# Kernel optimization log

Measured on AMD Instinct MI355X. Metric: run time of the kernel, lower is better.

## Reference

```python
import jax, jax.numpy as jnp
import numpy as np

D = 64        # input_dim == hidden dims
D2 = 2 * D    # transformer model dim
N = 20000     # num_nodes
R = 24        # num_relation
S = 3         # history snapshots
E = 60000     # edges per snapshot
B = 8         # batch
K = 101       # candidates (1 pos + 100 neg)
HLEN = 50     # history length
NL_GNN = 2
NL_TF = 2
NH = 2        # attention heads
HD = D2 // NH


def setup_inputs() -> dict:
    key = jax.random.key(0)
    ks = list(jax.random.split(key, 40))
    nrm = lambda i, shape: jax.random.normal(ks[i], shape, jnp.float32) * 0.05
    inp = {}
    # embeddings / params
    inp["poi_emb"] = nrm(0, (N, D))
    inp["query_emb"] = nrm(1, (R, D))
    inp["gate_W"] = nrm(2, (D, D)); inp["gate_b"] = jnp.zeros((D,), jnp.float32)
    inp["gnn_rel"] = nrm(3, (NL_GNN, R, D))
    inp["gnn_W"] = nrm(4, (NL_GNN, 2 * D, D)); inp["gnn_b"] = jnp.zeros((NL_GNN, D), jnp.float32)
    inp["g_time_emb"] = nrm(5, (48, D))
    inp["g_lin_W"] = nrm(6, (D, D)); inp["g_lin_b"] = jnp.zeros((D,), jnp.float32)
    inp["tf_Wqkv"] = nrm(7, (NL_TF, D2, 3 * D2))
    inp["tf_Wo"] = nrm(8, (NL_TF, D2, D2))
    ln = jnp.stack([jnp.ones((NL_TF, D2), jnp.float32), jnp.zeros((NL_TF, D2), jnp.float32)], axis=1)
    inp["tf_ln1"] = ln; inp["tf_ln2"] = ln
    inp["tf_W1"] = nrm(9, (NL_TF, D2, 4 * D2)); inp["tf_b1"] = jnp.zeros((NL_TF, 4 * D2), jnp.float32)
    inp["tf_W2"] = nrm(10, (NL_TF, 4 * D2, D2)); inp["tf_b2"] = jnp.zeros((NL_TF, D2), jnp.float32)
    F_DIM = D + D2  # hidden_dims[-1] + 2*input_dim
    inp["mlp_W1"] = nrm(11, (F_DIM, F_DIM)); inp["mlp_b1"] = jnp.zeros((F_DIM,), jnp.float32)
    inp["mlp_W2"] = nrm(12, (F_DIM, 1)); inp["mlp_b2"] = jnp.zeros((1,), jnp.float32)
    inp["history_time_encoding"] = nrm(13, (B, HLEN, D2))
    # graph / index inputs
    inp["edge_src"] = jax.random.randint(ks[14], (S, E), 0, N)
    inp["edge_dst"] = jax.random.randint(ks[15], (S, E), 0, N)
    inp["edge_type"] = jax.random.randint(ks[16], (S, E), 0, R)
    inp["h_index"] = jax.random.randint(ks[17], (B,), 0, N)
    inp["r_index"] = jax.random.randint(ks[18], (B,), 0, R)
    inp["t_index"] = jax.random.randint(ks[19], (B, K), 0, N)
    inp["history_poi"] = jax.random.randint(ks[20], (B, HLEN), 0, N)
    inp["g_time"] = jax.random.randint(ks[21], (S,), 0, 48)
    return inp


def _layer_norm(x, scale, bias):
    m = x.mean(-1, keepdims=True)
    v = ((x - m) ** 2).mean(-1, keepdims=True)
    return (x - m) * jax.lax.rsqrt(v + 1e-5) * scale + bias


def reference(poi_emb, query_emb, gate_W, gate_b, gnn_rel, gnn_W, gnn_b,
              g_time_emb, g_lin_W, g_lin_b,
              tf_Wqkv, tf_Wo, tf_ln1, tf_W1, tf_b1, tf_W2, tf_b2, tf_ln2,
              mlp_W1, mlp_b1, mlp_W2, mlp_b2,
              history_time_encoding,
              edge_src, edge_dst, edge_type, h_index, r_index, t_index,
              history_poi, g_time):
    query = query_emb[r_index]  # [B, D]  (r_index constant across candidates)
    output = jnp.zeros((B, N, D), poi_emb.dtype)
    for s in range(S):  # temporal snapshot loop (memory_update per snapshot)
        src, dst, et = edge_src[s], edge_dst[s], edge_type[s]
        # scatter_add of poi embeddings over both endpoints; identical per batch row
        poi_node = jnp.concatenate([src, dst])  # [2E]
        init_one = jax.ops.segment_sum(poi_emb[poi_node], poi_node, num_segments=N)  # [N, D]
        init = jnp.broadcast_to(init_one[None], (B, N, D))
        if s > 0:
            gate = jax.nn.sigmoid(output @ gate_W + gate_b)  # sigmoid gating vs prior state
            init = init * gate + (1.0 - gate) * output
        x = init
        for l in range(NL_GNN):  # PathAggNet stack: transe message + scatter-sum + linear
            msg = x[:, src] + gnn_rel[l][et][None]  # [B, E, D]
            agg = jnp.zeros((B, N, D), x.dtype).at[:, dst].add(msg)  # [B, N, D]
            x = jax.nn.relu(jnp.concatenate([agg, init], axis=-1) @ gnn_W[l] + gnn_b[l])
        output = x
        query = (query + g_time_emb[g_time[s]][None]) @ g_lin_W + g_lin_b
    feature = output  # [B, N, D]
    r_emb = jnp.broadcast_to(query[:, None], (B, N, D))
    final_feature = jnp.concatenate([feature, r_emb], axis=-1)  # [B, N, 2D]
    # gather history POI features + time encoding -> transformer encoder
    poi_idx = jnp.broadcast_to(history_poi[..., None], (B, HLEN, D2))
    xseq = jnp.take_along_axis(final_feature, poi_idx, axis=1) + history_time_encoding  # [B, HLEN, 2D]
    for l in range(NL_TF):
        qkv = xseq @ tf_Wqkv[l]  # [B, HLEN, 3*D2]
        q, k, v = jnp.split(qkv, 3, axis=-1)
        split_heads = lambda t: t.reshape(B, HLEN, NH, HD).transpose(0, 2, 1, 3)
        q, k, v = split_heads(q), split_heads(k), split_heads(v)
        att = jax.nn.softmax(jnp.einsum('bnqd,bnkd->bnqk', q, k) / jnp.sqrt(jnp.float32(HD)), axis=-1)
        o = jnp.einsum('bnqk,bnkd->bnqd', att, v).transpose(0, 2, 1, 3).reshape(B, HLEN, D2) @ tf_Wo[l]
        xseq = _layer_norm(xseq + o, tf_ln1[l, 0], tf_ln1[l, 1])
        ff = jax.nn.relu(xseq @ tf_W1[l] + tf_b1[l]) @ tf_W2[l] + tf_b2[l]
        xseq = _layer_norm(xseq + ff, tf_ln2[l, 0], tf_ln2[l, 1])
    feature_label = xseq.mean(axis=1, keepdims=True)  # [B, 1, 2D]
    t_idx = jnp.broadcast_to(t_index[..., None], (B, K, D))
    feature_t = jnp.take_along_axis(feature, t_idx, axis=1)  # [B, K, D]
    feature_t = jnp.concatenate([feature_t, jnp.broadcast_to(feature_label, (B, K, D2))], axis=-1)
    hmid = jax.nn.relu(feature_t @ mlp_W1 + mlp_b1)
    score = (hmid @ mlp_W2 + mlp_b2).squeeze(-1)  # [B, K]
    return score
```

## Files before the change

### kernel.cpp

```cpp
#include <hip/hip_runtime.h>
#include <hip/hip_bf16.h>
#include <math.h>

#define DD   64
#define DD2  128
#define NN   20000
#define RR   24
#define SS   3
#define EE   60000
#define BB   8
#define KK   101
#define HLENN 50
#define MROWS 20024

__global__ void hist_kernel(const int* __restrict__ src, const int* __restrict__ dst,
                            int* __restrict__ hist, int* __restrict__ deg) {
    int s = blockIdx.y;
    int e = blockIdx.x * 256 + threadIdx.x;
    if (e < EE) {
        int d0 = dst[s * EE + e], s0 = src[s * EE + e];
        atomicAdd(&hist[s * NN + d0], 1);
        atomicAdd(&deg[s * NN + d0], 1);
        atomicAdd(&deg[s * NN + s0], 1);
    }
}

__global__ void scan_kernel(const int* __restrict__ hist, int* __restrict__ rowptr,
                            int* __restrict__ cursor) {
    int s = blockIdx.x, t = threadIdx.x;
    const int* h = hist + s * NN;
    int* rp = rowptr + s * (NN + 1);
    int* cur = cursor + s * NN;
    __shared__ int sp[1024];
    int base = t * 20, sum = 0;
    for (int i = 0; i < 20; ++i) { int idx = base + i; if (idx < NN) sum += h[idx]; }
    sp[t] = sum;
    __syncthreads();
    for (int off = 1; off < 1024; off <<= 1) {
        int v = (t >= off) ? sp[t - off] : 0;
        __syncthreads();
        sp[t] += v;
        __syncthreads();
    }
    int run = sp[t] - sum;
    for (int i = 0; i < 20; ++i) {
        int idx = base + i;
        if (idx < NN) { rp[idx] = run; cur[idx] = run; run += h[idx]; }
    }
    if (t == 1023) rp[NN] = sp[1023];
}

__global__ void place_kernel(const int* __restrict__ src, const int* __restrict__ dst,
                             const int* __restrict__ et, int* __restrict__ cursor,
                             int* __restrict__ colp) {
    int s = blockIdx.y;
    int e = blockIdx.x * 256 + threadIdx.x;
    if (e < EE) {
        int d0 = dst[s * EE + e];
        int pos = atomicAdd(&cursor[s * NN + d0], 1);
        colp[s * EE + pos] = src[s * EE + e] | (et[s * EE + e] << 16);
    }
}

__global__ void init_kernel(const float* __restrict__ poi, const int* __restrict__ deg,
                            const float* __restrict__ gate_W, const float* __restrict__ gate_b,
                            const float* __restrict__ xprev, float* __restrict__ initb,
                            int use_gate) {
    __shared__ float sW[64][64];
    __shared__ float srow[4][64];
    int li = threadIdx.x >> 6, d = threadIdx.x & 63;
    int node = blockIdx.x * 4 + li;
    if (use_gate) {
        for (int i = threadIdx.x; i < 64 * 64; i += 256) sW[i >> 6][i & 63] = gate_W[i];
    }
    float iv = (float)deg[node] * poi[node * 64 + d];
    if (use_gate) {
        float ov = xprev[node * 64 + d];
        srow[li][d] = ov;
        __syncthreads();
        float acc = gate_b[d];
        #pragma unroll
        for (int k = 0; k < 64; ++k) acc += srow[li][k] * sW[k][d];
        float g = 1.f / (1.f + expf(-acc));
        iv = iv * g + (1.f - g) * ov;
    }
    initb[node * 64 + d] = iv;
}

__global__ void gemm64_kernel(const float* __restrict__ A0a, const float* __restrict__ Ar_a,
                              const float* __restrict__ Ba, float* __restrict__ Ca,
                              const float* __restrict__ A0b, const float* __restrict__ Ar_b,
                              const float* __restrict__ Bb, float* __restrict__ Cb) {
    const float* A0 = blockIdx.y ? A0b : A0a;
    const float* Ar = blockIdx.y ? Ar_b : Ar_a;
    const float* B  = blockIdx.y ? Bb  : Ba;
    float* C        = blockIdx.y ? Cb  : Ca;
    __shared__ float sA[64][68];
    __shared__ float sB[64][68];
    int tid = threadIdx.x;
    int row0 = blockIdx.x * 64;
    for (int i = tid; i < 64 * 16; i += 256) {
        int r = i >> 4, cq = i & 15;
        int row = row0 + r;
        float4 v = make_float4(0.f, 0.f, 0.f, 0.f);
        if (row < NN)        v = *(const float4*)(A0 + (size_t)row * 64 + cq * 4);
        else if (row < MROWS) v = *(const float4*)(Ar + (size_t)(row - NN) * 64 + cq * 4);
        *(float4*)&sA[r][cq * 4] = v;
        if (i < 64 * 16) {
            float4 w = *(const float4*)(B + (size_t)r * 64 + cq * 4);
            *(float4*)&sB[r][cq * 4] = w;
        }
    }
    __syncthreads();
    int tr = tid >> 4, tc = tid & 15;
    float acc[4][4] = {{0.f}};
    #pragma unroll 16
    for (int k = 0; k < 64; ++k) {
        float4 b4 = *(const float4*)&sB[k][tc * 4];
        float a0 = sA[tr * 4 + 0][k];
        float a1 = sA[tr * 4 + 1][k];
        float a2 = sA[tr * 4 + 2][k];
        float a3 = sA[tr * 4 + 3][k];
        acc[0][0] += a0 * b4.x; acc[0][1] += a0 * b4.y; acc[0][2] += a0 * b4.z; acc[0][3] += a0 * b4.w;
        acc[1][0] += a1 * b4.x; acc[1][1] += a1 * b4.y; acc[1][2] += a1 * b4.z; acc[1][3] += a1 * b4.w;
        acc[2][0] += a2 * b4.x; acc[2][1] += a2 * b4.y; acc[2][2] += a2 * b4.z; acc[2][3] += a2 * b4.w;
        acc[3][0] += a3 * b4.x; acc[3][1] += a3 * b4.y; acc[3][2] += a3 * b4.z; acc[3][3] += a3 * b4.w;
    }
    #pragma unroll
    for (int i = 0; i < 4; ++i) {
        int row = row0 + tr * 4 + i;
        if (row < MROWS) {
            float4 o = make_float4(acc[i][0], acc[i][1], acc[i][2], acc[i][3]);
            *(float4*)(C + (size_t)row * 64 + tc * 4) = o;
        }
    }
}

__global__ void fin_kernel(const float* __restrict__ y, const float* __restrict__ z,
                           const int* __restrict__ rowptr, const int* __restrict__ colp,
                           const float* __restrict__ bias, float* __restrict__ xout) {
    __shared__ float srelW[24][64];
    int tid = threadIdx.x;
    for (int i = tid; i < 24 * 64; i += 256) srelW[i >> 6][i & 63] = y[NN * 64 + i];
    int d = tid & 63, w = tid >> 6;
    float bb = bias[d];
    __syncthreads();
    int base = blockIdx.x * 16 + w * 4;
    for (int n = 0; n < 4; ++n) {
        int node = base + n;
        float acc = z[node * 64 + d] + bb;
        int e0 = rowptr[node], e1 = rowptr[node + 1];
        for (int e = e0; e < e1; ++e) {
            int pack = colp[e];
            acc += y[(size_t)(pack & 0xFFFF) * 64 + d] + srelW[pack >> 16][d];
        }
        xout[node * 64 + d] = fmaxf(acc, 0.f);
    }
}

__global__ void query_kernel(const float* __restrict__ query_emb, const int* __restrict__ r_index,
                             const float* __restrict__ g_time_emb, const int* __restrict__ g_time,
                             const float* __restrict__ g_lin_W, const float* __restrict__ g_lin_b,
                             float* __restrict__ query) {
    __shared__ float sW[64][64];
    __shared__ float sq[8][64];
    int b = threadIdx.x >> 6;
    int d = threadIdx.x & 63;
    for (int i = threadIdx.x; i < 64 * 64; i += 512) sW[i >> 6][i & 63] = g_lin_W[i];
    float q = query_emb[r_index[b] * 64 + d];
    for (int s = 0; s < SS; ++s) {
        float t = q + g_time_emb[g_time[s] * 64 + d];
        sq[b][d] = t;
        __syncthreads();
        float acc = g_lin_b[d];
        #pragma unroll
        for (int k = 0; k < 64; ++k) acc += sq[b][k] * sW[k][d];
        q = acc;
        __syncthreads();
    }
    query[b * 64 + d] = q;
}

__global__ void xseq_kernel(const float* __restrict__ feature, const float* __restrict__ query,
                            const int* __restrict__ history_poi, const float* __restrict__ hte,
                            float* __restrict__ xseq) {
    int idx = blockIdx.x * 256 + threadIdx.x;
    if (idx >= BB * HLENN * DD2) return;
    int c = idx & 127;
    int bt = idx >> 7;
    int b = bt / HLENN, t = bt % HLENN;
    float v = (c < 64) ? feature[history_poi[b * HLENN + t] * 64 + c]
                       : query[b * 64 + (c - 64)];
    xseq[idx] = v + hte[idx];
}

__global__ void qkv4_kernel(const float* __restrict__ xseq, const float* __restrict__ Wqkv,
                            float* __restrict__ qkvb) {
    __shared__ float sx[4][128];
    int tid = threadIdx.x;
    int row0 = blockIdx.x * 4;
    for (int i = tid; i < 512; i += 384) sx[i >> 7][i & 127] = xseq[row0 * 128 + i];
    __syncthreads();
    float a0 = 0.f, a1 = 0.f, a2 = 0.f, a3 = 0.f;
    #pragma unroll 8
    for (int k = 0; k < 128; ++k) {
        float w = Wqkv[k * 384 + tid];
        a0 += sx[0][k] * w; a1 += sx[1][k] * w; a2 += sx[2][k] * w; a3 += sx[3][k] * w;
    }
    qkvb[(row0 + 0) * 384 + tid] = a0;
    qkvb[(row0 + 1) * 384 + tid] = a1;
    qkvb[(row0 + 2) * 384 + tid] = a2;
    qkvb[(row0 + 3) * 384 + tid] = a3;
}

__global__ void attn_kernel(const float* __restrict__ qkv, float* __restrict__ attnout) {
    int b = blockIdx.x >> 1, h = blockIdx.x & 1;
    __shared__ float sq[HLENN][64], sk[HLENN][64], sv[HLENN][64];
    __shared__ float ss[HLENN][HLENN];
    for (int i = threadIdx.x; i < HLENN * 64; i += 256) {
        int t = i >> 6, d = i & 63;
        const float* base = qkv + (size_t)(b * HLENN + t) * 384 + h * 64 + d;
        sq[t][d] = base[0];
        sk[t][d] = base[128];
        sv[t][d] = base[256];
    }
    __syncthreads();
    for (int p = threadIdx.x; p < HLENN * HLENN; p += 256) {
        int i = p / HLENN, j = p % HLENN;
        float acc = 0.f;
        #pragma unroll 8
        for (int d = 0; d < 64; ++d) acc += sq[i][d] * sk[j][d];
        ss[i][j] = acc * 0.125f;
    }
    __syncthreads();
    if (threadIdx.x < HLENN) {
        int i = threadIdx.x;
        float m = -1e30f;
        for (int j = 0; j < HLENN; ++j) m = fmaxf(m, ss[i][j]);
        float sum = 0.f;
        for (int j = 0; j < HLENN; ++j) { float e = expf(ss[i][j] - m); ss[i][j] = e; sum += e; }
        float inv = 1.f / sum;
        for (int j = 0; j < HLENN; ++j) ss[i][j] *= inv;
    }
    __syncthreads();
    for (int p = threadIdx.x; p < HLENN * 64; p += 256) {
        int i = p >> 6, d = p & 63;
        float acc = 0.f;
        for (int j = 0; j < HLENN; ++j) acc += ss[i][j] * sv[j][d];
        attnout[(size_t)(b * HLENN + i) * 128 + h * 64 + d] = acc;
    }
}

__global__ void addLN4_kernel(const float* __restrict__ aout, const float* __restrict__ Wo,
                              const float* __restrict__ ln, float* __restrict__ xseq) {
    __shared__ float sa[4][128];
    __shared__ float sred[4][128];
    int tid = threadIdx.x;
    int r = tid >> 7, c = tid & 127;
    int row0 = blockIdx.x * 4;
    sa[r][c] = aout[(row0 + r) * 128 + c];
    __syncthreads();
    float acc = xseq[(row0 + r) * 128 + c];
    #pragma unroll 8
    for (int k = 0; k < 128; ++k) acc += sa[r][k] * Wo[k * 128 + c];
    sred[r][c] = acc; __syncthreads();
    for (int off = 64; off > 0; off >>= 1) { if (c < off) sred[r][c] += sred[r][c + off]; __syncthreads(); }
    float mean = sred[r][0] * (1.f / 128.f);
    __syncthreads();
    float dx = acc - mean;
    sred[r][c] = dx * dx; __syncthreads();
    for (int off = 64; off > 0; off >>= 1) { if (c < off) sred[r][c] += sred[r][c + off]; __syncthreads(); }
    float var = sred[r][0] * (1.f / 128.f);
    xseq[(row0 + r) * 128 + c] = dx * rsqrtf(var + 1e-5f) * ln[c] + ln[128 + c];
}

__global__ void ffLN4_kernel(const float* __restrict__ xin, const float* __restrict__ W1,
                             const float* __restrict__ b1, const float* __restrict__ W2,
                             const float* __restrict__ b2, const float* __restrict__ ln,
                             float* __restrict__ xout) {
    __shared__ float sx[4][128];
    __shared__ float sh[4][512];
    __shared__ float spart[4][4][128];
    __shared__ float sred[4][128];
    int tid = threadIdx.x;
    int row0 = blockIdx.x * 4;
    { int r = tid >> 7, c = tid & 127; sx[r][c] = xin[(row0 + r) * 128 + c]; }
    __syncthreads();
    {
        float bb = b1[tid];
        float a0 = bb, a1 = bb, a2 = bb, a3 = bb;
        #pragma unroll 8
        for (int k = 0; k < 128; ++k) {
            float w = W1[k * 512 + tid];
            a0 += sx[0][k] * w; a1 += sx[1][k] * w; a2 += sx[2][k] * w; a3 += sx[3][k] * w;
        }
        sh[0][tid] = fmaxf(a0, 0.f); sh[1][tid] = fmaxf(a1, 0.f);
        sh[2][tid] = fmaxf(a2, 0.f); sh[3][tid] = fmaxf(a3, 0.f);
    }
    __syncthreads();
    int kc = tid >> 7, c = tid & 127;
    float p0 = 0.f, p1 = 0.f, p2 = 0.f, p3 = 0.f;
    #pragma unroll 8
    for (int kk = 0; kk < 128; ++kk) {
        int k = kc * 128 + kk;
        float w = W2[k * 128 + c];
        p0 += sh[0][k] * w; p1 += sh[1][k] * w; p2 += sh[2][k] * w; p3 += sh[3][k] * w;
    }
    spart[kc][0][c] = p0; spart[kc][1][c] = p1; spart[kc][2][c] = p2; spart[kc][3][c] = p3;
    __syncthreads();
    int r = kc;
    float acc = b2[c] + spart[0][r][c] + spart[1][r][c] + spart[2][r][c] + spart[3][r][c] + sx[r][c];
    sred[r][c] = acc; __syncthreads();
    for (int off = 64; off > 0; off >>= 1) { if (c < off) sred[r][c] += sred[r][c + off]; __syncthreads(); }
    float mean = sred[r][0] * (1.f / 128.f);
    __syncthreads();
    float dx = acc - mean;
    sred[r][c] = dx * dx; __syncthreads();
    for (int off = 64; off > 0; off >>= 1) { if (c < off) sred[r][c] += sred[r][c + off]; __syncthreads(); }
    float var = sred[r][0] * (1.f / 128.f);
    xout[(row0 + r) * 128 + c] = dx * rsqrtf(var + 1e-5f) * ln[c] + ln[128 + c];
}

__global__ void mean_kernel(const float* __restrict__ xseq, float* __restrict__ flabel) {
    int i = blockIdx.x * 256 + threadIdx.x;
    if (i >= BB * 128) return;
    int b = i >> 7, c = i & 127;
    float s = 0.f;
    for (int t = 0; t < HLENN; ++t) s += xseq[(b * HLENN + t) * 128 + c];
    flabel[i] = s * (1.f / HLENN);
}

__global__ void score_kernel(const float* __restrict__ feature, const float* __restrict__ flabel,
                             const int* __restrict__ t_index,
                             const float* __restrict__ W1, const float* __restrict__ b1,
                             const float* __restrict__ W2, const float* __restrict__ b2,
                             float* __restrict__ score) {
    int b = blockIdx.x / KK, k = blockIdx.x % KK;
    __shared__ float sf[192];
    __shared__ float sred[192];
    int j = threadIdx.x;
    int t = t_index[b * KK + k];
    sf[j] = (j < 64) ? feature[t * 64 + j] : flabel[b * 128 + (j - 64)];
    __syncthreads();
    float acc = b1[j];
    #pragma unroll 8
    for (int i = 0; i < 192; ++i) acc += sf[i] * W1[i * 192 + j];
    float h = fmaxf(acc, 0.f);
    sred[j] = h * W2[j];
    __syncthreads();
    if (j < 64) sred[j] += sred[j + 64] + sred[j + 128];
    __syncthreads();
    for (int off = 32; off > 0; off >>= 1) { if (j < off) sred[j] += sred[j + off]; __syncthreads(); }
    if (j == 0) score[b * KK + k] = sred[0] + b2[0];
}

extern "C" void kernel_launch(void* const* d_in, const int* in_sizes, int n_in,
                              void* d_out, int out_size, void* d_ws, size_t ws_size,
                              hipStream_t stream) {
    const float* poi_emb   = (const float*)d_in[0];
    const float* query_emb = (const float*)d_in[1];
    const float* gate_W    = (const float*)d_in[2];
    const float* gate_b    = (const float*)d_in[3];
    const float* gnn_rel   = (const float*)d_in[4];
    const float* gnn_W     = (const float*)d_in[5];
    const float* gnn_b     = (const float*)d_in[6];
    const float* g_time_emb= (const float*)d_in[7];
    const float* g_lin_W   = (const float*)d_in[8];
    const float* g_lin_b   = (const float*)d_in[9];
    const float* tf_Wqkv   = (const float*)d_in[10];
    const float* tf_Wo     = (const float*)d_in[11];
    const float* tf_ln1    = (const float*)d_in[12];
    const float* tf_ln2    = (const float*)d_in[13];
    const float* tf_W1     = (const float*)d_in[14];
    const float* tf_b1     = (const float*)d_in[15];
    const float* tf_W2     = (const float*)d_in[16];
    const float* tf_b2     = (const float*)d_in[17];
    const float* mlp_W1    = (const float*)d_in[18];
    const float* mlp_b1    = (const float*)d_in[19];
    const float* mlp_W2    = (const float*)d_in[20];
    const float* mlp_b2    = (const float*)d_in[21];
    const float* hte       = (const float*)d_in[22];
    const int* edge_src    = (const int*)d_in[23];
    const int* edge_dst    = (const int*)d_in[24];
    const int* edge_type   = (const int*)d_in[25];
    const int* r_index     = (const int*)d_in[27];
    const int* t_index     = (const int*)d_in[28];
    const int* history_poi = (const int*)d_in[29];
    const int* g_time      = (const int*)d_in[30];

    float* ws = (float*)d_ws;
    float* xA    = ws;
    float* xB    = xA + 1280000;
    float* initb = xB + 1280000;
    float* y     = initb + 1280000;
    float* z     = y + 20032 * 64;
    float* query = z + 20032 * 64;
    float* xseq  = query + 512;
    float* qkvb  = xseq + 51200;
    float* aout  = qkvb + 153600;
    float* flab  = aout + 51200;
    int* hist    = (int*)(flab + 1024);
    int* deg     = hist + 3 * NN;
    int* rowptr  = deg + 3 * NN;
    int* cursor  = rowptr + 3 * (NN + 1);
    int* colp    = cursor + 3 * NN;

    hipMemsetAsync(hist, 0, 2 * 3 * NN * sizeof(int), stream);
    {
        dim3 g((EE + 255) / 256, 3);
        hist_kernel<<<g, 256, 0, stream>>>(edge_src, edge_dst, hist, deg);
        scan_kernel<<<3, 1024, 0, stream>>>(hist, rowptr, cursor);
        place_kernel<<<g, 256, 0, stream>>>(edge_src, edge_dst, edge_type, cursor, colp);
    }

    for (int s = 0; s < SS; ++s) {
        const int* rp = rowptr + s * (NN + 1);
        const int* cp = colp + s * EE;
        init_kernel<<<NN / 4, 256, 0, stream>>>(poi_emb, deg + s * NN, gate_W, gate_b,
                                                xA, initb, s > 0 ? 1 : 0);
        const float* Wt0 = gnn_W;
        const float* Wb0 = gnn_W + 64 * 64;
        const float* Wt1 = gnn_W + 128 * 64;
        const float* Wb1 = gnn_W + 128 * 64 + 64 * 64;
        const float* rel0 = gnn_rel;
        const float* rel1 = gnn_rel + 24 * 64;
        dim3 gg(313, 2);
        gemm64_kernel<<<gg, 256, 0, stream>>>(initb, rel0, Wt0, y,
                                              initb, rel0, Wb0, z);
        fin_kernel<<<NN / 16, 256, 0, stream>>>(y, z, rp, cp, gnn_b, xB);
        gemm64_kernel<<<gg, 256, 0, stream>>>(xB, rel1, Wt1, y,
                                              initb, rel1, Wb1, z);
        fin_kernel<<<NN / 16, 256, 0, stream>>>(y, z, rp, cp, gnn_b + 64, xA);
    }

    query_kernel<<<1, 512, 0, stream>>>(query_emb, r_index, g_time_emb, g_time,
                                        g_lin_W, g_lin_b, query);
    xseq_kernel<<<(BB * HLENN * 128 + 255) / 256, 256, 0, stream>>>(xA, query, history_poi, hte, xseq);

    for (int l = 0; l < 2; ++l) {
        qkv4_kernel<<<BB * HLENN / 4, 384, 0, stream>>>(xseq, tf_Wqkv + l * 128 * 384, qkvb);
        attn_kernel<<<BB * 2, 256, 0, stream>>>(qkvb, aout);
        addLN4_kernel<<<BB * HLENN / 4, 512, 0, stream>>>(aout, tf_Wo + l * 128 * 128,
                                                          tf_ln1 + l * 256, xseq);
        ffLN4_kernel<<<BB * HLENN / 4, 512, 0, stream>>>(xseq, tf_W1 + l * 128 * 512,
                                                         tf_b1 + l * 512, tf_W2 + l * 512 * 128,
                                                         tf_b2 + l * 128, tf_ln2 + l * 256, xseq);
    }

    mean_kernel<<<(BB * 128 + 255) / 256, 256, 0, stream>>>(xseq, flab);
    score_kernel<<<BB * KK, 192, 0, stream>>>(xA, flab, t_index,
                                              mlp_W1, mlp_b1, mlp_W2, mlp_b2, (float*)d_out);
}
```

Measured before the change: 526.0 us.

## Fuse CSR build, GNN init+GEMM, aggregation+GEMM, and transformer into few kernels

CSR construction now runs as a single per-snapshot kernel that uses an LDS histogram, scan and placement, replacing the memset and three launches. The gate/init step is fused with the dual y/z GEMM, and the first aggregation is fused with the next layer's GEMM, so intermediate node features are not round-tripped through global memory. The whole transformer, including the query chain, xseq build, two layers and the mean, runs in one kernel with one block per batch element. This cuts launch count and global traffic, at the cost of very low parallelism: the transformer uses only 8 blocks and the CSR build only 3 blocks with 1024 threads each.

```diff
diff --git a/kernel.cpp b/kernel.cpp
--- a/kernel.cpp
+++ b/kernel.cpp
@@ -13,27 +13,25 @@
 #define HLENN 50
 #define MROWS 20024
 
-__global__ void hist_kernel(const int* __restrict__ src, const int* __restrict__ dst,
-                            int* __restrict__ hist, int* __restrict__ deg) {
-    int s = blockIdx.y;
-    int e = blockIdx.x * 256 + threadIdx.x;
-    if (e < EE) {
-        int d0 = dst[s * EE + e], s0 = src[s * EE + e];
-        atomicAdd(&hist[s * NN + d0], 1);
-        atomicAdd(&deg[s * NN + d0], 1);
-        atomicAdd(&deg[s * NN + s0], 1);
-    }
-}
-
-__global__ void scan_kernel(const int* __restrict__ hist, int* __restrict__ rowptr,
-                            int* __restrict__ cursor) {
+__global__ __launch_bounds__(1024) void csr_kernel(
+        const int* __restrict__ src, const int* __restrict__ dst,
+        const int* __restrict__ et,
+        int* __restrict__ rowptr,
+        int* __restrict__ colp,
+        int* __restrict__ deg) {
+    __shared__ int lh[NN];
+    __shared__ int sp[1024];
     int s = blockIdx.x, t = threadIdx.x;
-    const int* h = hist + s * NN;
+    const int* ps = src + s * EE;
+    const int* pd = dst + s * EE;
+    const int* pt = et + s * EE;
     int* rp = rowptr + s * (NN + 1);
-    int* cur = cursor + s * NN;
-    __shared__ int sp[1024];
+    for (int i = t; i < NN; i += 1024) lh[i] = 0;
+    __syncthreads();
+    for (int e = t; e < EE; e += 1024) atomicAdd(&lh[pd[e]], 1);
+    __syncthreads();
     int base = t * 20, sum = 0;
-    for (int i = 0; i < 20; ++i) { int idx = base + i; if (idx < NN) sum += h[idx]; }
+    for (int i = 0; i < 20; ++i) { int idx = base + i; if (idx < NN) sum += lh[idx]; }
     sp[t] = sum;
     __syncthreads();
     for (int off = 1; off < 1024; off <<= 1) {
@@ -45,302 +43,352 @@
     int run = sp[t] - sum;
     for (int i = 0; i < 20; ++i) {
         int idx = base + i;
-        if (idx < NN) { rp[idx] = run; cur[idx] = run; run += h[idx]; }
+        if (idx < NN) { rp[idx] = run; int c = lh[idx]; lh[idx] = run; run += c; }
     }
     if (t == 1023) rp[NN] = sp[1023];
-}
-
-__global__ void place_kernel(const int* __restrict__ src, const int* __restrict__ dst,
-                             const int* __restrict__ et, int* __restrict__ cursor,
-                             int* __restrict__ colp) {
-    int s = blockIdx.y;
-    int e = blockIdx.x * 256 + threadIdx.x;
-    if (e < EE) {
-        int d0 = dst[s * EE + e];
-        int pos = atomicAdd(&cursor[s * NN + d0], 1);
-        colp[s * EE + pos] = src[s * EE + e] | (et[s * EE + e] << 16);
-    }
-}
-
-__global__ void init_kernel(const float* __restrict__ poi, const int* __restrict__ deg,
-                            const float* __restrict__ gate_W, const float* __restrict__ gate_b,
-                            const float* __restrict__ xprev, float* __restrict__ initb,
-                            int use_gate) {
-    __shared__ float sW[64][64];
+    __syncthreads();
+    for (int e = t; e < EE; e += 1024) {
+        int pos = atomicAdd(&lh[pd[e]], 1);
+        colp[s * EE + pos] = ps[e] | (pt[e] << 16);
+    }
+    __syncthreads();
+    for (int i = t; i < NN; i += 1024) lh[i] = 0;
+    __syncthreads();
+    for (int e = t; e < EE; e += 1024) atomicAdd(&lh[ps[e]], 1);
+    __syncthreads();
+    for (int i = t; i < NN; i += 1024)
+        deg[s * NN + i] = lh[i] + (rp[i + 1] - rp[i]);
+}
+
+__global__ __launch_bounds__(256) void initgemm_kernel(
+        const float* __restrict__ poi, const int* __restrict__ deg,
+        const float* __restrict__ gate_W, const float* __restrict__ gate_b,
+        const float* __restrict__ xprev, const float* __restrict__ rel,
+        const float* __restrict__ W,
+        float* __restrict__ initb, float* __restrict__ y, float* __restrict__ z,
+        int use_gate) {
+    __shared__ float sGW[64][64];
+    __shared__ float sA[64][68];
+    __shared__ float sBt[64][68];
+    __shared__ float sBb[64][68];
     __shared__ float srow[4][64];
-    int li = threadIdx.x >> 6, d = threadIdx.x & 63;
-    int node = blockIdx.x * 4 + li;
+    int tid = threadIdx.x;
+    int li = tid >> 6, d = tid & 63;
+    int row0 = blockIdx.x * 64;
     if (use_gate) {
-        for (int i = threadIdx.x; i < 64 * 64; i += 256) sW[i >> 6][i & 63] = gate_W[i];
-    }
-    float iv = (float)deg[node] * poi[node * 64 + d];
-    if (use_gate) {
-        float ov = xprev[node * 64 + d];
-        srow[li][d] = ov;
-        __syncthreads();
-        float acc = gate_b[d];
+        for (int i = tid; i < 64 * 64; i += 256) sGW[i >> 6][i & 63] = gate_W[i];
+        __syncthreads();
+    }
+    float gb = use_gate ? gate_b[d] : 0.f;
+    for (int it = 0; it < 16; ++it) {
+        int rl = it * 4 + li;
+        int row = row0 + rl;
+        float iv;
+        if (row < NN)           iv = (float)deg[row] * poi[(size_t)row * 64 + d];
+        else if (row < MROWS)   iv = rel[(row - NN) * 64 + d];
+        else                    iv = 0.f;
+        if (use_gate) {
+            float ov = (row < NN) ? xprev[(size_t)row * 64 + d] : 0.f;
+            srow[li][d] = ov;
+            __syncthreads();
+            float acc = gb;
+            #pragma unroll
+            for (int k = 0; k < 64; ++k) acc += srow[li][k] * sGW[k][d];
+            float g = 1.f / (1.f + expf(-acc));
+            if (row < NN) iv = iv * g + (1.f - g) * ov;
+            __syncthreads();
+        }
+        sA[rl][d] = iv;
+        if (row < NN) initb[(size_t)row * 64 + d] = iv;
+    }
+    for (int i = tid; i < 64 * 64; i += 256) {
+        sBt[i >> 6][i & 63] = W[i];
+        sBb[i >> 6][i & 63] = W[64 * 64 + i];
+    }
+    __syncthreads();
+    int tr = tid >> 4, tc = tid & 15;
+    float accY[4][4] = {{0.f}}, accZ[4][4] = {{0.f}};
+    #pragma unroll 16
+    for (int k = 0; k < 64; ++k) {
+        float4 bt = *(const float4*)&sBt[k][tc * 4];
+        float4 bz = *(const float4*)&sBb[k][tc * 4];
         #pragma unroll
-        for (int k = 0; k < 64; ++k) acc += srow[li][k] * sW[k][d];
-        float g = 1.f / (1.f + expf(-acc));
-        iv = iv * g + (1.f - g) * ov;
-    }
-    initb[node * 64 + d] = iv;
-}
-
-__global__ void gemm64_kernel(const float* __restrict__ A0a, const float* __restrict__ Ar_a,
-                              const float* __restrict__ Ba, float* __restrict__ Ca,
-                              const float* __restrict__ A0b, const float* __restrict__ Ar_b,
-                              const float* __restrict__ Bb, float* __restrict__ Cb) {
-    const float* A0 = blockIdx.y ? A0b : A0a;
-    const float* Ar = blockIdx.y ? Ar_b : Ar_a;
-    const float* B  = blockIdx.y ? Bb  : Ba;
-    float* C        = blockIdx.y ? Cb  : Ca;
+        for (int i = 0; i < 4; ++i) {
+            float a = sA[tr * 4 + i][k];
+            accY[i][0] += a * bt.x; accY[i][1] += a * bt.y; accY[i][2] += a * bt.z; accY[i][3] += a * bt.w;
+            accZ[i][0] += a * bz.x; accZ[i][1] += a * bz.y; accZ[i][2] += a * bz.z; accZ[i][3] += a * bz.w;
+        }
+    }
+    #pragma unroll
+    for (int i = 0; i < 4; ++i) {
+        int row = row0 + tr * 4 + i;
+        if (row < MROWS) {
+            *(float4*)(y + (size_t)row * 64 + tc * 4) = make_float4(accY[i][0], accY[i][1], accY[i][2], accY[i][3]);
+            *(float4*)(z + (size_t)row * 64 + tc * 4) = make_float4(accZ[i][0], accZ[i][1], accZ[i][2], accZ[i][3]);
+        }
+    }
+}
+
+__global__ __launch_bounds__(256) void fingemm_kernel(
+        const float* __restrict__ y, const float* __restrict__ z,
+        const int* __restrict__ rp, const int* __restrict__ cp,
+        const float* __restrict__ bias0, const float* __restrict__ rel1,
+        const float* __restrict__ W1,
+        const float* __restrict__ initb,
+        float* __restrict__ y2, float* __restrict__ z2) {
+    __shared__ float srelW[24][64];
     __shared__ float sA[64][68];
-    __shared__ float sB[64][68];
+    __shared__ float sAi[64][68];
+    __shared__ float sBt[64][68];
+    __shared__ float sBb[64][68];
     int tid = threadIdx.x;
+    int li = tid >> 6, d = tid & 63;
     int row0 = blockIdx.x * 64;
+    for (int i = tid; i < 24 * 64; i += 256) srelW[i >> 6][i & 63] = y[(size_t)NN * 64 + i];
+    for (int i = tid; i < 64 * 64; i += 256) {
+        sBt[i >> 6][i & 63] = W1[i];
+        sBb[i >> 6][i & 63] = W1[64 * 64 + i];
+    }
     for (int i = tid; i < 64 * 16; i += 256) {
         int r = i >> 4, cq = i & 15;
         int row = row0 + r;
         float4 v = make_float4(0.f, 0.f, 0.f, 0.f);
-        if (row < NN)        v = *(const float4*)(A0 + (size_t)row * 64 + cq * 4);
-        else if (row < MROWS) v = *(const float4*)(Ar + (size_t)(row - NN) * 64 + cq * 4);
-        *(float4*)&sA[r][cq * 4] = v;
-        if (i < 64 * 16) {
-            float4 w = *(const float4*)(B + (size_t)r * 64 + cq * 4);
-            *(float4*)&sB[r][cq * 4] = w;
-        }
+        if (row < NN) v = *(const float4*)(initb + (size_t)row * 64 + cq * 4);
+        *(float4*)&sAi[r][cq * 4] = v;
+    }
+    __syncthreads();
+    float bb0 = bias0[d];
+    for (int it = 0; it < 16; ++it) {
+        int rl = it * 4 + li;
+        int row = row0 + rl;
+        float val = 0.f;
+        if (row < NN) {
+            float acc = z[(size_t)row * 64 + d] + bb0;
+            int e0 = rp[row], e1 = rp[row + 1];
+            for (int e = e0; e < e1; ++e) {
+                int pack = cp[e];
+                acc += y[(size_t)(pack & 0xFFFF) * 64 + d] + srelW[pack >> 16][d];
+            }
+            val = fmaxf(acc, 0.f);
+        } else if (row < MROWS) {
+            val = rel1[(row - NN) * 64 + d];
+        }
+        sA[rl][d] = val;
     }
     __syncthreads();
     int tr = tid >> 4, tc = tid & 15;
-    float acc[4][4] = {{0.f}};
+    float accY[4][4] = {{0.f}}, accZ[4][4] = {{0.f}};
     #pragma unroll 16
     for (int k = 0; k < 64; ++k) {
-        float4 b4 = *(const float4*)&sB[k][tc * 4];
-        float a0 = sA[tr * 4 + 0][k];
-        float a1 = sA[tr * 4 + 1][k];
-        float a2 = sA[tr * 4 + 2][k];
-        float a3 = sA[tr * 4 + 3][k];
-        acc[0][0] += a0 * b4.x; acc[0][1] += a0 * b4.y; acc[0][2] += a0 * b4.z; acc[0][3] += a0 * b4.w;
-        acc[1][0] += a1 * b4.x; acc[1][1] += a1 * b4.y; acc[1][2] += a1 * b4.z; acc[1][3] += a1 * b4.w;
-        acc[2][0] += a2 * b4.x; acc[2][1] += a2 * b4.y; acc[2][2] += a2 * b4.z; acc[2][3] += a2 * b4.w;
-        acc[3][0] += a3 * b4.x; acc[3][1] += a3 * b4.y; acc[3][2] += a3 * b4.z; acc[3][3] += a3 * b4.w;
+        float4 bt = *(const float4*)&sBt[k][tc * 4];
+        float4 bz = *(const float4*)&sBb[k][tc * 4];
+        #pragma unroll
+        for (int i = 0; i < 4; ++i) {
+            float a  = sA[tr * 4 + i][k];
+            float ai = sAi[tr * 4 + i][k];
+            accY[i][0] += a * bt.x;  accY[i][1] += a * bt.y;  accY[i][2] += a * bt.z;  accY[i][3] += a * bt.w;
+            accZ[i][0] += ai * bz.x; accZ[i][1] += ai * bz.y; accZ[i][2] += ai * bz.z; accZ[i][3] += ai * bz.w;
+        }
     }
     #pragma unroll
     for (int i = 0; i < 4; ++i) {
         int row = row0 + tr * 4 + i;
         if (row < MROWS) {
-            float4 o = make_float4(acc[i][0], acc[i][1], acc[i][2], acc[i][3]);
-            *(float4*)(C + (size_t)row * 64 + tc * 4) = o;
-        }
-    }
-}
-
-__global__ void fin_kernel(const float* __restrict__ y, const float* __restrict__ z,
-                           const int* __restrict__ rowptr, const int* __restrict__ colp,
-                           const float* __restrict__ bias, float* __restrict__ xout) {
+            *(float4*)(y2 + (size_t)row * 64 + tc * 4) = make_float4(accY[i][0], accY[i][1], accY[i][2], accY[i][3]);
+            *(float4*)(z2 + (size_t)row * 64 + tc * 4) = make_float4(accZ[i][0], accZ[i][1], accZ[i][2], accZ[i][3]);
+        }
+    }
+}
+
+__global__ __launch_bounds__(256) void fin_kernel(
+        const float* __restrict__ y, const float* __restrict__ z,
+        const int* __restrict__ rowptr, const int* __restrict__ colp,
+        const float* __restrict__ bias, float* __restrict__ xout) {
     __shared__ float srelW[24][64];
     int tid = threadIdx.x;
-    for (int i = tid; i < 24 * 64; i += 256) srelW[i >> 6][i & 63] = y[NN * 64 + i];
+    for (int i = tid; i < 24 * 64; i += 256) srelW[i >> 6][i & 63] = y[(size_t)NN * 64 + i];
     int d = tid & 63, w = tid >> 6;
     float bb = bias[d];
     __syncthreads();
     int base = blockIdx.x * 16 + w * 4;
     for (int n = 0; n < 4; ++n) {
         int node = base + n;
-        float acc = z[node * 64 + d] + bb;
+        float acc = z[(size_t)node * 64 + d] + bb;
         int e0 = rowptr[node], e1 = rowptr[node + 1];
         for (int e = e0; e < e1; ++e) {
             int pack = colp[e];
             acc += y[(size_t)(pack & 0xFFFF) * 64 + d] + srelW[pack >> 16][d];
         }
-        xout[node * 64 + d] = fmaxf(acc, 0.f);
-    }
-}
-
-__global__ void query_kernel(const float* __restrict__ query_emb, const int* __restrict__ r_index,
-                             const float* __restrict__ g_time_emb, const int* __restrict__ g_time,
-                             const float* __restrict__ g_lin_W, const float* __restrict__ g_lin_b,
-                             float* __restrict__ query) {
-    __shared__ float sW[64][64];
-    __shared__ float sq[8][64];
-    int b = threadIdx.x >> 6;
-    int d = threadIdx.x & 63;
-    for (int i = threadIdx.x; i < 64 * 64; i += 512) sW[i >> 6][i & 63] = g_lin_W[i];
-    float q = query_emb[r_index[b] * 64 + d];
+        xout[(size_t)node * 64 + d] = fmaxf(acc, 0.f);
+    }
+}
+
+__global__ __launch_bounds__(512) void tf_kernel(
+        const float* __restrict__ feature, const float* __restrict__ query_emb,
+        const int* __restrict__ r_index, const float* __restrict__ g_time_emb,
+        const int* __restrict__ g_time, const float* __restrict__ g_lin_W,
+        const float* __restrict__ g_lin_b, const int* __restrict__ history_poi,
+        const float* __restrict__ hte,
+        const float* __restrict__ tf_Wqkv, const float* __restrict__ tf_Wo,
+        const float* __restrict__ tf_ln1, const float* __restrict__ tf_ln2,
+        const float* __restrict__ tf_W1, const float* __restrict__ tf_b1,
+        const float* __restrict__ tf_W2, const float* __restrict__ tf_b2,
+        float* __restrict__ flab) {
+    __shared__ float sxseq[HLENN][128];
+    __shared__ float sbig[25600];
+    __shared__ float ss[2][HLENN][HLENN];
+    __shared__ float sq[64], sq2[64];
+    __shared__ float smean[HLENN], svar[HLENN];
+    int b = blockIdx.x, tid = threadIdx.x;
+    if (tid < 64) sq2[tid] = query_emb[r_index[b] * 64 + tid];
+    __syncthreads();
     for (int s = 0; s < SS; ++s) {
-        float t = q + g_time_emb[g_time[s] * 64 + d];
-        sq[b][d] = t;
-        __syncthreads();
-        float acc = g_lin_b[d];
+        if (tid < 64) sq[tid] = sq2[tid] + g_time_emb[g_time[s] * 64 + tid];
+        __syncthreads();
+        float acc = 0.f;
+        if (tid < 64) {
+            acc = g_lin_b[tid];
+            #pragma unroll 8
+            for (int k = 0; k < 64; ++k) acc += sq[k] * g_lin_W[k * 64 + tid];
+        }
+        __syncthreads();
+        if (tid < 64) sq2[tid] = acc;
+        __syncthreads();
+    }
+    for (int p = tid; p < HLENN * 128; p += 512) {
+        int t = p >> 7, c = p & 127;
+        float v = (c < 64) ? feature[(size_t)history_poi[b * HLENN + t] * 64 + c]
+                           : sq2[c - 64];
+        sxseq[t][c] = v + hte[(b * HLENN + t) * 128 + c];
+    }
+    __syncthreads();
+    for (int l = 0; l < 2; ++l) {
+        const float* Wqkv = tf_Wqkv + l * 128 * 384;
+        const float* Wo   = tf_Wo   + l * 128 * 128;
+        const float* W1   = tf_W1   + l * 128 * 512;
+        const float* b1   = tf_b1   + l * 512;
+        const float* W2   = tf_W2   + l * 512 * 128;
+        const float* b2   = tf_b2   + l * 128;
+        const float* ln1  = tf_ln1  + l * 256;
+        const float* ln2  = tf_ln2  + l * 256;
+        for (int p = tid; p < HLENN * 384; p += 512) {
+            int t = p / 384, j = p % 384;
+            float acc = 0.f;
+            #pragma unroll 8
+            for (int k = 0; k < 128; ++k) acc += sxseq[t][k] * Wqkv[k * 384 + j];
+            sbig[t * 384 + j] = acc;
+        }
+        __syncthreads();
+        for (int p = tid; p < 2 * HLENN * HLENN; p += 512) {
+            int h = p / 2500, r = (p / 50) % 50, j = p % 50;
+            float acc = 0.f;
+            #pragma unroll 8
+            for (int k = 0; k < 64; ++k)
+                acc += sbig[r * 384 + h * 64 + k] * sbig[j * 384 + 128 + h * 64 + k];
+            ss[h][r][j] = acc * 0.125f;
+        }
+        __syncthreads();
+        if (tid < 2 * HLENN) {
+            int h = tid / HLENN, r = tid % HLENN;
+            float m = -1e30f;
+            for (int j = 0; j < HLENN; ++j) m = fmaxf(m, ss[h][r][j]);
+            float sum = 0.f;
+            for (int j = 0; j < HLENN; ++j) { float e = expf(ss[h][r][j] - m); ss[h][r][j] = e; sum += e; }
+            float inv = 1.f / sum;
+            for (int j = 0; j < HLENN; ++j) ss[h][r][j] *= inv;
+        }
+        __syncthreads();
+        for (int p = tid; p < HLENN * 128; p += 512) {
+            int t = p >> 7, c = p & 127, h = c >> 6, cc = c & 63;
+            float acc = 0.f;
+            for (int j = 0; j < HLENN; ++j)
+                acc += ss[h][t][j] * sbig[j * 384 + 256 + h * 64 + cc];
+            sbig[19200 + p] = acc;
+        }
+        __syncthreads();
+        for (int p = tid; p < HLENN * 128; p += 512) {
+            int t = p >> 7, c = p & 127;
+            float acc = sxseq[t][c];
+            #pragma unroll 8
+            for (int k = 0; k < 128; ++k) acc += sbig[19200 + t * 128 + k] * Wo[k * 128 + c];
+            sbig[p] = acc;
+        }
+        __syncthreads();
+        if (tid < HLENN) {
+            float m = 0.f;
+            for (int k = 0; k < 128; ++k) m += sbig[tid * 128 + k];
+            m *= (1.f / 128.f);
+            float v = 0.f;
+            for (int k = 0; k < 128; ++k) { float dx = sbig[tid * 128 + k] - m; v += dx * dx; }
+            smean[tid] = m; svar[tid] = v * (1.f / 128.f);
+        }
+        __syncthreads();
+        for (int p = tid; p < HLENN * 128; p += 512) {
+            int t = p >> 7, c = p & 127;
+            sxseq[t][c] = (sbig[p] - smean[t]) * rsqrtf(svar[t] + 1e-5f) * ln1[c] + ln1[128 + c];
+        }
+        __syncthreads();
+        for (int p = tid; p < HLENN * 512; p += 512) {
+            int t = p >> 9, j = p & 511;
+            float acc = b1[j];
+            #pragma unroll 8
+            for (int k = 0; k < 128; ++k) acc += sxseq[t][k] * W1[k * 512 + j];
+            sbig[p] = fmaxf(acc, 0.f);
+        }
+        __syncthreads();
+        float r2[13];
         #pragma unroll
-        for (int k = 0; k < 64; ++k) acc += sq[b][k] * sW[k][d];
-        q = acc;
-        __syncthreads();
-    }
-    query[b * 64 + d] = q;
-}
-
-__global__ void xseq_kernel(const float* __restrict__ feature, const float* __restrict__ query,
-                            const int* __restrict__ history_poi, const float* __restrict__ hte,
-                            float* __restrict__ xseq) {
-    int idx = blockIdx.x * 256 + threadIdx.x;
-    if (idx >= BB * HLENN * DD2) return;
-    int c = idx & 127;
-    int bt = idx >> 7;
-    int b = bt / HLENN, t = bt % HLENN;
-    float v = (c < 64) ? feature[history_poi[b * HLENN + t] * 64 + c]
-                       : query[b * 64 + (c - 64)];
-    xseq[idx] = v + hte[idx];
-}
-
-__global__ void qkv4_kernel(const float* __restrict__ xseq, const float* __restrict__ Wqkv,
-                            float* __restrict__ qkvb) {
-    __shared__ float sx[4][128];
-    int tid = threadIdx.x;
-    int row0 = blockIdx.x * 4;
-    for (int i = tid; i < 512; i += 384) sx[i >> 7][i & 127] = xseq[row0 * 128 + i];
-    __syncthreads();
-    float a0 = 0.f, a1 = 0.f, a2 = 0.f, a3 = 0.f;
-    #pragma unroll 8
-    for (int k = 0; k < 128; ++k) {
-        float w = Wqkv[k * 384 + tid];
-        a0 += sx[0][k] * w; a1 += sx[1][k] * w; a2 += sx[2][k] * w; a3 += sx[3][k] * w;
-    }
-    qkvb[(row0 + 0) * 384 + tid] = a0;
-    qkvb[(row0 + 1) * 384 + tid] = a1;
-    qkvb[(row0 + 2) * 384 + tid] = a2;
-    qkvb[(row0 + 3) * 384 + tid] = a3;
-}
-
-__global__ void attn_kernel(const float* __restrict__ qkv, float* __restrict__ attnout) {
-    int b = blockIdx.x >> 1, h = blockIdx.x & 1;
-    __shared__ float sq[HLENN][64], sk[HLENN][64], sv[HLENN][64];
-    __shared__ float ss[HLENN][HLENN];
-    for (int i = threadIdx.x; i < HLENN * 64; i += 256) {
-        int t = i >> 6, d = i & 63;
-        const float* base = qkv + (size_t)(b * HLENN + t) * 384 + h * 64 + d;
-        sq[t][d] = base[0];
-        sk[t][d] = base[128];
-        sv[t][d] = base[256];
-    }
-    __syncthreads();
-    for (int p = threadIdx.x; p < HLENN * HLENN; p += 256) {
-        int i = p / HLENN, j = p % HLENN;
-        float acc = 0.f;
-        #pragma unroll 8
-        for (int d = 0; d < 64; ++d) acc += sq[i][d] * sk[j][d];
-        ss[i][j] = acc * 0.125f;
-    }
-    __syncthreads();
-    if (threadIdx.x < HLENN) {
-        int i = threadIdx.x;
-        float m = -1e30f;
-        for (int j = 0; j < HLENN; ++j) m = fmaxf(m, ss[i][j]);
-        float sum = 0.f;
-        for (int j = 0; j < HLENN; ++j) { float e = expf(ss[i][j] - m); ss[i][j] = e; sum += e; }
-        float inv = 1.f / sum;
-        for (int j = 0; j < HLENN; ++j) ss[i][j] *= inv;
-    }
-    __syncthreads();
-    for (int p = threadIdx.x; p < HLENN * 64; p += 256) {
-        int i = p >> 6, d = p & 63;
-        float acc = 0.f;
-        for (int j = 0; j < HLENN; ++j) acc += ss[i][j] * sv[j][d];
-        attnout[(size_t)(b * HLENN + i) * 128 + h * 64 + d] = acc;
-    }
-}
-
-__global__ void addLN4_kernel(const float* __restrict__ aout, const float* __restrict__ Wo,
-                              const float* __restrict__ ln, float* __restrict__ xseq) {
-    __shared__ float sa[4][128];
-    __shared__ float sred[4][128];
-    int tid = threadIdx.x;
-    int r = tid >> 7, c = tid & 127;
-    int row0 = blockIdx.x * 4;
-    sa[r][c] = aout[(row0 + r) * 128 + c];
-    __syncthreads();
-    float acc = xseq[(row0 + r) * 128 + c];
-    #pragma unroll 8
-    for (int k = 0; k < 128; ++k) acc += sa[r][k] * Wo[k * 128 + c];
-    sred[r][c] = acc; __syncthreads();
-    for (int off = 64; off > 0; off >>= 1) { if (c < off) sred[r][c] += sred[r][c + off]; __syncthreads(); }
-    float mean = sred[r][0] * (1.f / 128.f);
-    __syncthreads();
-    float dx = acc - mean;
-    sred[r][c] = dx * dx; __syncthreads();
-    for (int off = 64; off > 0; off >>= 1) { if (c < off) sred[r][c] += sred[r][c + off]; __syncthreads(); }
-    float var = sred[r][0] * (1.f / 128.f);
-    xseq[(row0 + r) * 128 + c] = dx * rsqrtf(var + 1e-5f) * ln[c] + ln[128 + c];
-}
-
-__global__ void ffLN4_kernel(const float* __restrict__ xin, const float* __restrict__ W1,
-                             const float* __restrict__ b1, const float* __restrict__ W2,
-                             const float* __restrict__ b2, const float* __restrict__ ln,
-                             float* __restrict__ xout) {
-    __shared__ float sx[4][128];
-    __shared__ float sh[4][512];
-    __shared__ float spart[4][4][128];
-    __shared__ float sred[4][128];
-    int tid = threadIdx.x;
-    int row0 = blockIdx.x * 4;
-    { int r = tid >> 7, c = tid & 127; sx[r][c] = xin[(row0 + r) * 128 + c]; }
-    __syncthreads();
-    {
-        float bb = b1[tid];
-        float a0 = bb, a1 = bb, a2 = bb, a3 = bb;
-        #pragma unroll 8
-        for (int k = 0; k < 128; ++k) {
-            float w = W1[k * 512 + tid];
-            a0 += sx[0][k] * w; a1 += sx[1][k] * w; a2 += sx[2][k] * w; a3 += sx[3][k] * w;
-        }
-        sh[0][tid] = fmaxf(a0, 0.f); sh[1][tid] = fmaxf(a1, 0.f);
-        sh[2][tid] = fmaxf(a2, 0.f); sh[3][tid] = fmaxf(a3, 0.f);
-    }
-    __syncthreads();
-    int kc = tid >> 7, c = tid & 127;
-    float p0 = 0.f, p1 = 0.f, p2 = 0.f, p3 = 0.f;
-    #pragma unroll 8
-    for (int kk = 0; kk < 128; ++kk) {
-        int k = kc * 128 + kk;
-        float w = W2[k * 128 + c];
-        p0 += sh[0][k] * w; p1 += sh[1][k] * w; p2 += sh[2][k] * w; p3 += sh[3][k] * w;
-    }
-    spart[kc][0][c] = p0; spart[kc][1][c] = p1; spart[kc][2][c] = p2; spart[kc][3][c] = p3;
-    __syncthreads();
-    int r = kc;
-    float acc = b2[c] + spart[0][r][c] + spart[1][r][c] + spart[2][r][c] + spart[3][r][c] + sx[r][c];
-    sred[r][c] = acc; __syncthreads();
-    for (int off = 64; off > 0; off >>= 1) { if (c < off) sred[r][c] += sred[r][c + off]; __syncthreads(); }
-    float mean = sred[r][0] * (1.f / 128.f);
-    __syncthreads();
-    float dx = acc - mean;
-    sred[r][c] = dx * dx; __syncthreads();
-    for (int off = 64; off > 0; off >>= 1) { if (c < off) sred[r][c] += sred[r][c + off]; __syncthreads(); }
-    float var = sred[r][0] * (1.f / 128.f);
-    xout[(row0 + r) * 128 + c] = dx * rsqrtf(var + 1e-5f) * ln[c] + ln[128 + c];
-}
-
-__global__ void mean_kernel(const float* __restrict__ xseq, float* __restrict__ flabel) {
-    int i = blockIdx.x * 256 + threadIdx.x;
-    if (i >= BB * 128) return;
-    int b = i >> 7, c = i & 127;
-    float s = 0.f;
-    for (int t = 0; t < HLENN; ++t) s += xseq[(b * HLENN + t) * 128 + c];
-    flabel[i] = s * (1.f / HLENN);
-}
-
-__global__ void score_kernel(const float* __restrict__ feature, const float* __restrict__ flabel,
-                             const int* __restrict__ t_index,
-                             const float* __restrict__ W1, const float* __restrict__ b1,
-                             const float* __restrict__ W2, const float* __restrict__ b2,
-                             float* __restrict__ score) {
+        for (int i = 0; i < 13; ++i) {
+            int p = tid + i * 512;
+            if (p < HLENN * 128) {
+                int t = p >> 7, c = p & 127;
+                float acc = b2[c] + sxseq[t][c];
+                #pragma unroll 8
+                for (int k = 0; k < 512; ++k) acc += sbig[t * 512 + k] * W2[k * 128 + c];
+                r2[i] = acc;
+            }
+        }
+        __syncthreads();
+        #pragma unroll
+        for (int i = 0; i < 13; ++i) {
+            int p = tid + i * 512;
+            if (p < HLENN * 128) sbig[p] = r2[i];
+        }
+        __syncthreads();
+        if (tid < HLENN) {
+            float m = 0.f;
+            for (int k = 0; k < 128; ++k) m += sbig[tid * 128 + k];
+            m *= (1.f / 128.f);
+            float v = 0.f;
+            for (int k = 0; k < 128; ++k) { float dx = sbig[tid * 128 + k] - m; v += dx * dx; }
+            smean[tid] = m; svar[tid] = v * (1.f / 128.f);
+        }
+        __syncthreads();
+        for (int p = tid; p < HLENN * 128; p += 512) {
+            int t = p >> 7, c = p & 127;
+            sxseq[t][c] = (sbig[p] - smean[t]) * rsqrtf(svar[t] + 1e-5f) * ln2[c] + ln2[128 + c];
+        }
+        __syncthreads();
+    }
+    if (tid < 128) {
+        float s = 0.f;
+        for (int t = 0; t < HLENN; ++t) s += sxseq[t][tid];
+        flab[b * 128 + tid] = s * (1.f / HLENN);
+    }
+}
+
+__global__ __launch_bounds__(192) void score_kernel(
+        const float* __restrict__ feature, const float* __restrict__ flabel,
+        const int* __restrict__ t_index,
+        const float* __restrict__ W1, const float* __restrict__ b1,
+        const float* __restrict__ W2, const float* __restrict__ b2,
+        float* __restrict__ score) {
     int b = blockIdx.x / KK, k = blockIdx.x % KK;
     __shared__ float sf[192];
     __shared__ float sred[192];
     int j = threadIdx.x;
     int t = t_index[b * KK + k];
-    sf[j] = (j < 64) ? feature[t * 64 + j] : flabel[b * 128 + (j - 64)];
+    sf[j] = (j < 64) ? feature[(size_t)t * 64 + j] : flabel[b * 128 + (j - 64)];
     __syncthreads();
     float acc = b1[j];
     #pragma unroll 8
@@ -390,64 +438,41 @@
 
     float* ws = (float*)d_ws;
     float* xA    = ws;
-    float* xB    = xA + 1280000;
-    float* initb = xB + 1280000;
+    float* initb = xA    + 1280000;
     float* y     = initb + 1280000;
-    float* z     = y + 20032 * 64;
-    float* query = z + 20032 * 64;
-    float* xseq  = query + 512;
-    float* qkvb  = xseq + 51200;
-    float* aout  = qkvb + 153600;
-    float* flab  = aout + 51200;
-    int* hist    = (int*)(flab + 1024);
-    int* deg     = hist + 3 * NN;
-    int* rowptr  = deg + 3 * NN;
-    int* cursor  = rowptr + 3 * (NN + 1);
-    int* colp    = cursor + 3 * NN;
-
-    hipMemsetAsync(hist, 0, 2 * 3 * NN * sizeof(int), stream);
-    {
-        dim3 g((EE + 255) / 256, 3);
-        hist_kernel<<<g, 256, 0, stream>>>(edge_src, edge_dst, hist, deg);
-        scan_kernel<<<3, 1024, 0, stream>>>(hist, rowptr, cursor);
-        place_kernel<<<g, 256, 0, stream>>>(edge_src, edge_dst, edge_type, cursor, colp);
-    }
+    float* z     = y     + 1282048;
+    float* y2    = z     + 1282048;
+    float* z2    = y2    + 1282048;
+    float* flab  = z2    + 1282048;
+    int* rowptr  = (int*)(flab + 1024);
+    int* colp    = rowptr + 3 * (NN + 1);
+    int* deg     = colp + 3 * EE;
+
+    csr_kernel<<<3, 1024, 0, stream>>>(edge_src, edge_dst, edge_type,
+                                       rowptr, colp, deg);
 
     for (int s = 0; s < SS; ++s) {
         const int* rp = rowptr + s * (NN + 1);
         const int* cp = colp + s * EE;
-        init_kernel<<<NN / 4, 256, 0, stream>>>(poi_emb, deg + s * NN, gate_W, gate_b,
-                                                xA, initb, s > 0 ? 1 : 0);
-        const float* Wt0 = gnn_W;
-        const float* Wb0 = gnn_W + 64 * 64;
-        const float* Wt1 = gnn_W + 128 * 64;
-        const float* Wb1 = gnn_W + 128 * 64 + 64 * 64;
-        const float* rel0 = gnn_rel;
-        const float* rel1 = gnn_rel + 24 * 64;
-        dim3 gg(313, 2);
-        gemm64_kernel<<<gg, 256, 0, stream>>>(initb, rel0, Wt0, y,
-                                              initb, rel0, Wb0, z);
-        fin_kernel<<<NN / 16, 256, 0, stream>>>(y, z, rp, cp, gnn_b, xB);
-        gemm64_kernel<<<gg, 256, 0, stream>>>(xB, rel1, Wt1, y,
-                                              initb, rel1, Wb1, z);
-        fin_kernel<<<NN / 16, 256, 0, stream>>>(y, z, rp, cp, gnn_b + 64, xA);
-    }
-
-    query_kernel<<<1, 512, 0, stream>>>(query_emb, r_index, g_time_emb, g_time,
-                                        g_lin_W, g_lin_b, query);
-    xseq_kernel<<<(BB * HLENN * 128 + 255) / 256, 256, 0, stream>>>(xA, query, history_poi, hte, xseq);
-
-    for (int l = 0; l < 2; ++l) {
-        qkv4_kernel<<<BB * HLENN / 4, 384, 0, stream>>>(xseq, tf_Wqkv + l * 128 * 384, qkvb);
-        attn_kernel<<<BB * 2, 256, 0, stream>>>(qkvb, aout);
-        addLN4_kernel<<<BB * HLENN / 4, 512, 0, stream>>>(aout, tf_Wo + l * 128 * 128,
-                                                          tf_ln1 + l * 256, xseq);
-        ffLN4_kernel<<<BB * HLENN / 4, 512, 0, stream>>>(xseq, tf_W1 + l * 128 * 512,
-                                                         tf_b1 + l * 512, tf_W2 + l * 512 * 128,
-                                                         tf_b2 + l * 128, tf_ln2 + l * 256, xseq);
-    }
-
-    mean_kernel<<<(BB * 128 + 255) / 256, 256, 0, stream>>>(xseq, flab);
+        initgemm_kernel<<<313, 256, 0, stream>>>(
+            poi_emb, deg + s * NN, gate_W, gate_b, xA,
+            gnn_rel,
+            gnn_W,
+            initb, y, z, s > 0 ? 1 : 0);
+        fingemm_kernel<<<313, 256, 0, stream>>>(
+            y, z, rp, cp, gnn_b,
+            gnn_rel + 24 * 64,
+            gnn_W + 128 * 64,
+            initb, y2, z2);
+        fin_kernel<<<NN / 16, 256, 0, stream>>>(y2, z2, rp, cp, gnn_b + 64, xA);
+    }
+
+    tf_kernel<<<BB, 512, 0, stream>>>(
+        xA, query_emb, r_index, g_time_emb, g_time, g_lin_W, g_lin_b,
+        history_poi, hte, tf_Wqkv, tf_Wo, tf_ln1, tf_ln2,
+        tf_W1, tf_b1, tf_W2, tf_b2, flab);
+
     score_kernel<<<BB * KK, 192, 0, stream>>>(xA, flab, t_index,
-                                              mlp_W1, mlp_b1, mlp_W2, mlp_b2, (float*)d_out);
-}
+                                              mlp_W1, mlp_b1, mlp_W2, mlp_b2,
+                                              (float*)d_out);
+}
```

Result: slower. 1.462 ms (+177.9%).
